# Optimization experiments

Hardware: AMD Instinct MI355X
Metric: run time of the kernel (lower is better)

Reference implementation:

```python
import jax, jax.numpy as jnp
import numpy as np

QN = 127.0  # 2^(8-1)-1, symmetric int8
EPS = 1e-5  # batchnorm eps

def ste_round(v):
    return v + jax.lax.stop_gradient(jnp.round(v) - v)

def quant_act(x):
    # HAWQ-style symmetric per-tensor activation quantization (8-bit)
    s = jnp.maximum(jnp.max(jnp.abs(x)) / QN, 1e-8)
    xq = jnp.clip(ste_round(x / s), -QN - 1.0, QN)
    return xq * s, s

def setup_inputs() -> dict:
    key = jax.random.key(0)
    k1, k2, k3, k4, k5, k6 = jax.random.split(key, 6)
    B, Cin, Cout, H, W = 128, 768, 192, 17, 17
    x = jax.random.normal(k1, (B, Cin, H, W), dtype=jnp.float32)
    conv_w = jax.random.normal(k2, (Cout, Cin, 1, 1), dtype=jnp.float32) * 0.02
    bn_gamma = 1.0 + 0.1 * jax.random.normal(k3, (Cout,), dtype=jnp.float32)
    bn_beta = 0.1 * jax.random.normal(k4, (Cout,), dtype=jnp.float32)
    bn_mean = 0.1 * jax.random.normal(k5, (Cout,), dtype=jnp.float32)
    bn_var = 0.5 + jax.random.uniform(k6, (Cout,), dtype=jnp.float32)
    return {"x": x, "conv_w": conv_w, "bn_gamma": bn_gamma, "bn_beta": bn_beta,
            "bn_mean": bn_mean, "bn_var": bn_var, "cluster": 0}

def reference(x, conv_w, bn_gamma, bn_beta, bn_mean, bn_var, cluster):
    # 1) QuantAct on raw input
    x1, s0 = quant_act(x)
    # 2) QuantAveragePool2d (k=3, s=1, p=1, count_include_pad=True): pool in integer domain
    x_int = ste_round(x1 / s0)
    pooled_sum = jax.lax.reduce_window(x_int, 0.0, jax.lax.add,
                                       (1, 1, 3, 3), (1, 1, 1, 1),
                                       [(0, 0), (0, 0), (1, 1), (1, 1)])
    x2 = (pooled_sum / 9.0) * s0
    # 3) QuantAct after pool
    x3, s1 = quant_act(x2)
    # 4) QuantBnConv2d: fold BN into 1x1 conv, per-channel symmetric weight quant
    std = jnp.sqrt(bn_var + EPS)
    w_fold = conv_w * (bn_gamma / std)[:, None, None, None]          # [O,C,1,1]
    b_fold = bn_beta - bn_gamma * bn_mean / std                      # [O]
    w_sf = jnp.maximum(jnp.max(jnp.abs(w_fold), axis=(1, 2, 3)) / QN, 1e-8)  # [O]
    w_int = jnp.clip(ste_round(w_fold / w_sf[:, None, None, None]), -QN - 1.0, QN)
    xi = x3 / s1                                                     # integer-valued acts
    b_int = ste_round(b_fold / (w_sf * s1))
    out_int = jnp.einsum('bchw,oc->bohw', xi, w_int[:, :, 0, 0]) + b_int[None, :, None, None]
    out = out_int * (w_sf * s1)[None, :, None, None]
    # 5) ReLU + output QuantAct
    out = jax.nn.relu(out)
    outq, s2 = quant_act(out)
    return outq, s2
```

## Files before the change

### kernel.cpp

```cpp
#include <hip/hip_runtime.h>
#include <math.h>

#define B_    128
#define C_    768
#define O_    192
#define HW_   289
#define N_IN  (128*768*289)
#define N_OUT (128*192*289)
#define QN_   127.0f

#define SLAB_E   (32*289)
#define SLAB_SH  9248
#define SLAB_BYT 18496
#define QP_LDS   (32*380)

#define AB_BLOCKS 2048

typedef __attribute__((ext_vector_type(4))) int i32x4;

#define SWZ(b) ((b) ^ ((((b) >> 6) & 3) << 4))


__global__ void k_pre(const float4* __restrict__ x4, int n4,
                      const float* __restrict__ conv_w,
                      const float* __restrict__ g,
                      const float* __restrict__ beta,
                      const float* __restrict__ mu,
                      const float* __restrict__ var,
                      signed char* __restrict__ w_q8,
                      float* __restrict__ wsf_g, float* __restrict__ bf_g,
                      unsigned* cnt) {
    if (blockIdx.x < AB_BLOCKS) {
        float m = 0.f;
        const int stride = AB_BLOCKS * blockDim.x;
        int i = blockIdx.x * blockDim.x + threadIdx.x;
        for (; i + stride < n4; i += 2 * stride) {
            float4 v = x4[i];
            float4 w = x4[i + stride];
            m = fmaxf(m, fmaxf(fmaxf(fabsf(v.x), fabsf(v.y)),
                               fmaxf(fabsf(v.z), fabsf(v.w))));
            m = fmaxf(m, fmaxf(fmaxf(fabsf(w.x), fabsf(w.y)),
                               fmaxf(fabsf(w.z), fabsf(w.w))));
        }
        if (i < n4) {
            float4 v = x4[i];
            m = fmaxf(m, fmaxf(fmaxf(fabsf(v.x), fabsf(v.y)),
                               fmaxf(fabsf(v.z), fabsf(v.w))));
        }
#pragma unroll
        for (int off = 32; off; off >>= 1) m = fmaxf(m, __shfl_down(m, off));
        __shared__ float sm[4];
        int lane = threadIdx.x & 63, wv = threadIdx.x >> 6;
        if (lane == 0) sm[wv] = m;
        __syncthreads();
        if (threadIdx.x == 0) {
            float bm = fmaxf(fmaxf(sm[0], sm[1]), fmaxf(sm[2], sm[3]));
            atomicMax(cnt + 0, __float_as_uint(bm));
        }
        return;
    }
    const int o = blockIdx.x - AB_BLOCKS;
    const float stdv = sqrtf(var[o] + 1e-5f);
    const float r = g[o] / stdv;
    const float* wo = conv_w + o * C_;
    float m = 0.f;
    for (int c = threadIdx.x; c < C_; c += 256) m = fmaxf(m, fabsf(wo[c] * r));
#pragma unroll
    for (int off = 32; off; off >>= 1) m = fmaxf(m, __shfl_down(m, off));
    __shared__ float sm2[4];
    __shared__ float swsf;
    int lane = threadIdx.x & 63, wv = threadIdx.x >> 6;
    if (lane == 0) sm2[wv] = m;
    __syncthreads();
    if (threadIdx.x == 0) {
        float bm = fmaxf(fmaxf(sm2[0], sm2[1]), fmaxf(sm2[2], sm2[3]));
        swsf = fmaxf(bm / QN_, 1e-8f);
    }
    __syncthreads();
    const float wsf = swsf;
    for (int c = threadIdx.x; c < C_; c += 256) {
        float wi = rintf(wo[c] * r / wsf);
        wi = fminf(fmaxf(wi, -128.f), 127.f);
        w_q8[(c >> 6) * 12288 + o * 64 + (c & 63)] = (signed char)(int)wi;
    }
    if (threadIdx.x == 0) {
        wsf_g[o] = wsf;
        bf_g[o] = beta[o] - g[o] * mu[o] / stdv;
    }
}

__launch_bounds__(512) __global__
void k_quant_pool(const float* __restrict__ x, short* __restrict__ pooled,
                  unsigned* cnt) {
    __shared__ __align__(16) float fq[QP_LDS + 8];
    __shared__ int smax[8];
    const int tid = threadIdx.x;
    const int kt = blockIdx.x;
    const int b = blockIdx.z;
    const float s0 = fmaxf(__uint_as_float(cnt[0]) / QN_, 1e-8f);

    for (int i = tid; i < 32 * 91; i += 512) {
        int p = i / 91, rem = i - p * 91;
        int slot;
        if (rem < 20) slot = rem;
        else if (rem < 40) slot = 360 + (rem - 20);
        else {
            int t = rem - 40;
            int rr = t / 3, cc = t - rr * 3;
            slot = (rr + 1) * 20 + (cc == 0 ? 0 : 17 + cc);
        }
        fq[p * 380 + slot] = 0.f;
    }
    if (tid < 8) fq[QP_LDS + tid] = 0.f;

    const float4* xg4 = (const float4*)(x + ((size_t)b * 768 + kt * 32) * HW_);
    for (int t = tid; t < SLAB_E / 4; t += 512) {
        float4 v = xg4[t];
        float q0 = rintf(v.x / s0);
        float q1 = rintf(v.y / s0);
        float q2 = rintf(v.z / s0);
        float q3 = rintf(v.w / s0);
        int e = 4 * t;
#pragma unroll
        for (int j = 0; j < 4; ++j) {
            float q = (j == 0) ? q0 : (j == 1) ? q1 : (j == 2) ? q2 : q3;
            int ej = e + j;
            int p = (ej * 29027) >> 23;
            int i2 = ej - p * 289;
            int r = (i2 * 3856) >> 16;
            int c = i2 - r * 17;
            fq[p * 380 + (r + 1) * 20 + (c + 1)] = q;
        }
    }
    __syncthreads();

    short* slab = pooled + (size_t)(b * 24 + kt) * SLAB_SH;
    int tmax = 0;
    for (int task = tid; task < 2720; task += 512) {
        int p = task & 31;
        int rt = task >> 5;
        int r = (rt * 3277) >> 14;
        int t5 = rt - r * 5;
        int c0 = t5 * 4;
        const float* base = fq + p * 380 + r * 20 + c0;
        float4 a0 = *(const float4*)(base);
        float4 a1 = *(const float4*)(base + 4);
        float4 b0 = *(const float4*)(base + 20);
        float4 b1 = *(const float4*)(base + 24);
        float4 d0 = *(const float4*)(base + 40);
        float4 d1 = *(const float4*)(base + 44);
        float s0c = a0.x + b0.x + d0.x;
        float s1c = a0.y + b0.y + d0.y;
        float s2c = a0.z + b0.z + d0.z;
        float s3c = a0.w + b0.w + d0.w;
        float s4c = a1.x + b1.x + d1.x;
        float s5c = a1.y + b1.y + d1.y;
        int o0 = (int)(s0c + s1c + s2c);
        int o1 = (int)(s1c + s2c + s3c);
        int o2 = (int)(s2c + s3c + s4c);
        int o3 = (int)(s3c + s4c + s5c);
        int i0 = r * 17 + c0;
        slab[(i0 + 0) * 32 + p] = (short)o0;
        int a = o0 < 0 ? -o0 : o0; tmax = a > tmax ? a : tmax;
        if (c0 + 1 < 17) {
            slab[(i0 + 1) * 32 + p] = (short)o1;
            a = o1 < 0 ? -o1 : o1; tmax = a > tmax ? a : tmax;
            slab[(i0 + 2) * 32 + p] = (short)o2;
            a = o2 < 0 ? -o2 : o2; tmax = a > tmax ? a : tmax;
            slab[(i0 + 3) * 32 + p] = (short)o3;
            a = o3 < 0 ? -o3 : o3; tmax = a > tmax ? a : tmax;
        }
    }

#pragma unroll
    for (int off = 32; off; off >>= 1) {
        int o = __shfl_down(tmax, off);
        tmax = o > tmax ? o : tmax;
    }
    if ((tid & 63) == 0) smax[tid >> 6] = tmax;
    __syncthreads();
    if (tid == 0) {
        int bm = smax[0];
#pragma unroll
        for (int i = 1; i < 8; ++i) bm = smax[i] > bm ? smax[i] : bm;
        atomicMax((int*)(cnt + 1), bm);
    }
}

__launch_bounds__(256) __global__
void k_gemm(const short* __restrict__ pooled,
            const signed char* __restrict__ w_q8,
            const float* __restrict__ wsf_g, const float* __restrict__ bf_g,
            unsigned* cnt, float* __restrict__ out) {
    __shared__ char sW[2][12288];
    __shared__ char sX[2][5120];
    __shared__ unsigned char s_lut[2305];
    __shared__ float s_bint[192];
    __shared__ float s_scale[192];
    __shared__ float red[4];
    const int tid = threadIdx.x;
    const int b = blockIdx.z;
    const int hw0 = blockIdx.x * 80;
    const int L = tid & 63;
    const int wv = tid >> 6;
    const int wo = wv * 48;
    const char* pooled_b = (const char*)pooled;

    {
        const float s0 = fmaxf(__uint_as_float(cnt[0]) / QN_, 1e-8f);
        const float maxx2 = ((float)((const int*)cnt)[1] / 9.0f) * s0;
        const float s1 = fmaxf(maxx2 / QN_, 1e-8f);
        for (int i = tid; i < 2305; i += 256) {
            float p = (float)(i - 1152);
            float t = (p / 9.0f) * s0;
            float v = rintf(t / s1);
            v = fminf(fmaxf(v, -128.f), 127.f);
            s_lut[i] = (unsigned char)(signed char)(int)v;
        }
        if (tid < 192) {
            float wsf = wsf_g[tid];
            s_bint[tid] = rintf(bf_g[tid] / (wsf * s1));
            s_scale[tid] = wsf * s1;
        }
    }

    const int row0 = tid >> 3, ch0 = tid & 7;
    const int row1 = 32 + (tid >> 3), ch1 = tid & 7;
    const int row2 = 64 + (tid >> 3), ch2 = tid & 7;
    const bool act2 = tid < 128;

    uint4 xr0, xr1, xr2;

    auto stageW = [&](int kt, int buf) {
#pragma unroll
        for (int j = 0; j < 3; ++j) {
            int ldsoff = (wv * 3 + j) * 1024;
            const char* src = (const char*)w_q8 + kt * 12288 + SWZ(ldsoff + L * 16);
            __builtin_amdgcn_global_load_lds(
                (const __attribute__((address_space(1))) unsigned int*)src,
                (__attribute__((address_space(3))) unsigned int*)(&sW[buf][0] + ldsoff),
                16, 0, 0);
        }
    };
    auto ldx = [&](int kt, int row, int ch) -> uint4 {
        uint4 z; z.x = z.y = z.z = z.w = 0u;
        int hw = hw0 + row;
        if (hw >= HW_) return z;
        size_t slab = (size_t)(b * 24 + 2 * kt + (ch >> 2)) * SLAB_BYT;
        return *(const uint4*)(pooled_b + slab + hw * 64 + (ch & 3) * 16);
    };
    auto loadX = [&](int kt) {
        xr0 = ldx(kt, row0, ch0);
        xr1 = ldx(kt, row1, ch1);
        if (act2) xr2 = ldx(kt, row2, ch2);
    };
    auto pack8 = [&](const uint4& v) -> uint2 {
        unsigned c0 = s_lut[1152 + (short)(v.x)];
        unsigned c1 = s_lut[1152 + (short)(v.x >> 16)];
        unsigned c2 = s_lut[1152 + (short)(v.y)];
        unsigned c3 = s_lut[1152 + (short)(v.y >> 16)];
        unsigned c4 = s_lut[1152 + (short)(v.z)];
        unsigned c5 = s_lut[1152 + (short)(v.z >> 16)];
        unsigned c6 = s_lut[1152 + (short)(v.w)];
        unsigned c7 = s_lut[1152 + (short)(v.w >> 16)];
        uint2 r;
        r.x = c0 | (c1 << 8) | (c2 << 16) | (c3 << 24);
        r.y = c4 | (c5 << 8) | (c6 << 16) | (c7 << 24);
        return r;
    };
    auto writeX = [&](int buf) {
        *(uint2*)(&sX[buf][0] + SWZ(row0 * 64 + ch0 * 8)) = pack8(xr0);
        *(uint2*)(&sX[buf][0] + SWZ(row1 * 64 + ch1 * 8)) = pack8(xr1);
        if (act2) *(uint2*)(&sX[buf][0] + SWZ(row2 * 64 + ch2 * 8)) = pack8(xr2);
    };

    i32x4 acc[3][5] = {};

    stageW(0, 0);
    loadX(0);
    __syncthreads();
    writeX(0);
    __syncthreads();

    for (int kt = 0; kt < 12; ++kt) {
        const int cur = kt & 1, nxt = cur ^ 1;
        if (kt < 11) {
            stageW(kt + 1, nxt);
            loadX(kt + 1);
        }
        i32x4 af[3], bfr[5];
#pragma unroll
        for (int m = 0; m < 3; ++m)
            af[m] = *(const i32x4*)(&sW[cur][0] +
                SWZ((wo + m * 16 + (L & 15)) * 64 + (L >> 4) * 16));
#pragma unroll
        for (int n = 0; n < 5; ++n)
            bfr[n] = *(const i32x4*)(&sX[cur][0] +
                SWZ((n * 16 + (L & 15)) * 64 + (L >> 4) * 16));
#pragma unroll
        for (int m = 0; m < 3; ++m)
#pragma unroll
            for (int n = 0; n < 5; ++n)
                acc[m][n] = __builtin_amdgcn_mfma_i32_16x16x64_i8(
                    af[m], bfr[n], acc[m][n], 0, 0, 0);
        if (kt < 11) writeX(nxt);
        __syncthreads();
    }

    float lmax = 0.f;
#pragma unroll
    for (int m = 0; m < 3; ++m) {
        int ob = wo + m * 16 + (L >> 4) * 4;
        float bi0 = s_bint[ob + 0], bi1 = s_bint[ob + 1];
        float bi2 = s_bint[ob + 2], bi3 = s_bint[ob + 3];
        float sc0 = s_scale[ob + 0], sc1 = s_scale[ob + 1];
        float sc2 = s_scale[ob + 2], sc3 = s_scale[ob + 3];
#pragma unroll
        for (int n = 0; n < 5; ++n) {
            int hw = hw0 + n * 16 + (L & 15);
            if (hw < HW_) {
                size_t base = ((size_t)b * O_ + ob) * HW_ + hw;
                float v0 = fmaxf(((float)acc[m][n][0] + bi0) * sc0, 0.f);
                float v1 = fmaxf(((float)acc[m][n][1] + bi1) * sc1, 0.f);
                float v2 = fmaxf(((float)acc[m][n][2] + bi2) * sc2, 0.f);
                float v3 = fmaxf(((float)acc[m][n][3] + bi3) * sc3, 0.f);
                out[base + 0 * HW_] = v0;
                out[base + 1 * HW_] = v1;
                out[base + 2 * HW_] = v2;
                out[base + 3 * HW_] = v3;
                lmax = fmaxf(fmaxf(fmaxf(v0, v1), fmaxf(v2, v3)), lmax);
            }
        }
    }
#pragma unroll
    for (int off = 32; off; off >>= 1) lmax = fmaxf(lmax, __shfl_down(lmax, off));
    if (L == 0) red[wv] = lmax;
    __syncthreads();
    if (tid == 0) {
        float bm = fmaxf(fmaxf(red[0], red[1]), fmaxf(red[2], red[3]));
        atomicMax(cnt + 2, __float_as_uint(bm));
    }
}

__global__ void k_quant_out(float* __restrict__ out, const unsigned* __restrict__ cnt) {
    const float s2 = fmaxf(__uint_as_float(cnt[2]) / QN_, 1e-8f);
    float4* o4 = (float4*)out;
    const int n4 = N_OUT / 4;
    for (int i = blockIdx.x * blockDim.x + threadIdx.x; i < n4;
         i += gridDim.x * blockDim.x) {
        float4 v = o4[i];
        v.x = fminf(fmaxf(rintf(v.x / s2), -128.f), 127.f) * s2;
        v.y = fminf(fmaxf(rintf(v.y / s2), -128.f), 127.f) * s2;
        v.z = fminf(fmaxf(rintf(v.z / s2), -128.f), 127.f) * s2;
        v.w = fminf(fmaxf(rintf(v.w / s2), -128.f), 127.f) * s2;
        o4[i] = v;
    }
    if (blockIdx.x == 0 && threadIdx.x == 0) out[N_OUT] = s2;
}

extern "C" void kernel_launch(void* const* d_in, const int* in_sizes, int n_in,
                              void* d_out, int out_size, void* d_ws, size_t ws_size,
                              hipStream_t stream) {
    const float* x      = (const float*)d_in[0];
    const float* conv_w = (const float*)d_in[1];
    const float* g      = (const float*)d_in[2];
    const float* beta   = (const float*)d_in[3];
    const float* mu     = (const float*)d_in[4];
    const float* var    = (const float*)d_in[5];
    float* out = (float*)d_out;

    char* wsb = (char*)d_ws;
    unsigned* cnt          = (unsigned*)wsb;
    float* wsf_g           = (float*)(wsb + 4096);
    float* bf_g            = (float*)(wsb + 5120);
    signed char* w_q8      = (signed char*)(wsb + 8192);
    short* pooled          = (short*)(wsb + (1u << 20));

    hipMemsetAsync(cnt, 0, 16, stream);
    k_pre<<<AB_BLOCKS + O_, 256, 0, stream>>>((const float4*)x, N_IN / 4, conv_w,
                                              g, beta, mu, var, w_q8, wsf_g, bf_g,
                                              cnt);
    dim3 qgrid(24, 1, B_);
    k_quant_pool<<<qgrid, 512, 0, stream>>>(x, pooled, cnt);
    dim3 ggrid(4, 1, B_);
    k_gemm<<<ggrid, 256, 0, stream>>>(pooled, w_q8, wsf_g, bf_g, cnt, out);
    k_quant_out<<<2048, 256, 0, stream>>>(out, cnt);
}
```

Baseline: 126.7 us.

## Split quant+pool into int8 quantize pass and separate LDS pool kernel

Replaces the fused quantize-and-pool kernel with two kernels. A grid-stride kernel quantizes x to int8 and writes it into the back half of each pooled slab. A second kernel loads that int8 slab into LDS and computes the 3x3 integer box sum with byte-unpacking and edge masking, writing int16 results in place. This shrinks LDS use and raises occupancy, at the cost of an extra launch and an extra global round trip of the int8 data, plus in-place aliasing between the int8 region and the int16 output.

```diff
diff --git a/kernel.cpp b/kernel.cpp
--- a/kernel.cpp
+++ b/kernel.cpp
@@ -9,11 +9,8 @@
 #define N_OUT (128*192*289)
 #define QN_   127.0f
 
-#define SLAB_E   (32*289)
 #define SLAB_SH  9248
 #define SLAB_BYT 18496
-#define QP_LDS   (32*380)
-
 #define AB_BLOCKS 2048
 
 typedef __attribute__((ext_vector_type(4))) int i32x4;
@@ -89,85 +86,114 @@
     }
 }
 
-__launch_bounds__(512) __global__
-void k_quant_pool(const float* __restrict__ x, short* __restrict__ pooled,
-                  unsigned* cnt) {
-    __shared__ __align__(16) float fq[QP_LDS + 8];
-    __shared__ int smax[8];
+__global__ void k_quant(const float4* __restrict__ x4, char* __restrict__ pbase,
+                        const unsigned* __restrict__ cnt) {
+    const float s0 = fmaxf(__uint_as_float(cnt[0]) / QN_, 1e-8f);
+    const int n4 = N_IN / 4;
+    for (int t = blockIdx.x * blockDim.x + threadIdx.x; t < n4;
+         t += gridDim.x * blockDim.x) {
+        float4 v = x4[t];
+        int q0 = (int)rintf(v.x / s0);
+        int q1 = (int)rintf(v.y / s0);
+        int q2 = (int)rintf(v.z / s0);
+        int q3 = (int)rintf(v.w / s0);
+        int e = 4 * t;
+        unsigned gp = (unsigned)e / 289u;
+        int hw = e - (int)gp * 289;
+        if (hw <= 285) {
+            size_t off = (size_t)(gp >> 5) * SLAB_BYT + 9248 + (gp & 31) * 289 + hw;
+            unsigned pk = (q0 & 0xff) | ((q1 & 0xff) << 8) | ((q2 & 0xff) << 16) |
+                          ((unsigned)(q3 & 0xff) << 24);
+            *(unsigned*)(pbase + off) = pk;
+        } else {
+            int qs0 = q0, qs1 = q1, qs2 = q2, qs3 = q3;
+#pragma unroll
+            for (int j = 0; j < 4; ++j) {
+                int qv = (j == 0) ? qs0 : (j == 1) ? qs1 : (j == 2) ? qs2 : qs3;
+                int ej = e + j;
+                unsigned gj = (unsigned)ej / 289u;
+                int hwj = ej - (int)gj * 289;
+                size_t oj = (size_t)(gj >> 5) * SLAB_BYT + 9248 + (gj & 31) * 289 + hwj;
+                pbase[oj] = (char)qv;
+            }
+        }
+    }
+}
+
+__launch_bounds__(256) __global__
+void k_pool(short* __restrict__ pooled, unsigned* cnt) {
+    __shared__ __align__(4) char sq[4 + 9248 + 12];
+    __shared__ int smax[4];
     const int tid = threadIdx.x;
-    const int kt = blockIdx.x;
-    const int b = blockIdx.z;
-    const float s0 = fmaxf(__uint_as_float(cnt[0]) / QN_, 1e-8f);
-
-    for (int i = tid; i < 32 * 91; i += 512) {
-        int p = i / 91, rem = i - p * 91;
-        int slot;
-        if (rem < 20) slot = rem;
-        else if (rem < 40) slot = 360 + (rem - 20);
-        else {
-            int t = rem - 40;
-            int rr = t / 3, cc = t - rr * 3;
-            slot = (rr + 1) * 20 + (cc == 0 ? 0 : 17 + cc);
-        }
-        fq[p * 380 + slot] = 0.f;
-    }
-    if (tid < 8) fq[QP_LDS + tid] = 0.f;
-
-    const float4* xg4 = (const float4*)(x + ((size_t)b * 768 + kt * 32) * HW_);
-    for (int t = tid; t < SLAB_E / 4; t += 512) {
-        float4 v = xg4[t];
-        float q0 = rintf(v.x / s0);
-        float q1 = rintf(v.y / s0);
-        float q2 = rintf(v.z / s0);
-        float q3 = rintf(v.w / s0);
-        int e = 4 * t;
-#pragma unroll
-        for (int j = 0; j < 4; ++j) {
-            float q = (j == 0) ? q0 : (j == 1) ? q1 : (j == 2) ? q2 : q3;
-            int ej = e + j;
-            int p = (ej * 29027) >> 23;
-            int i2 = ej - p * 289;
-            int r = (i2 * 3856) >> 16;
-            int c = i2 - r * 17;
-            fq[p * 380 + (r + 1) * 20 + (c + 1)] = q;
-        }
-    }
-    __syncthreads();
-
-    short* slab = pooled + (size_t)(b * 24 + kt) * SLAB_SH;
+    const int s = blockIdx.x;
+    char* region = (char*)pooled + (size_t)s * SLAB_BYT;
+
+    {
+        const unsigned* src = (const unsigned*)(region + 9248);
+        unsigned* dst = (unsigned*)(sq + 4);
+        for (int i = tid; i < 2312; i += 256) dst[i] = src[i];
+    }
+    if (tid < 4) *(unsigned*)(sq + tid * 4 * 0) = 0;
+    if (tid < 3) *(unsigned*)(sq + 4 + 9248 + tid * 4) = 0;
+    __syncthreads();
+
+    auto load6 = [&](int off, int& b0, int& b1, int& b2, int& b3, int& b4,
+                     int& b5) {
+        int al = off & ~3;
+        const char* base = sq + 4 + al;
+        unsigned w0 = *(const unsigned*)(base);
+        unsigned w1 = *(const unsigned*)(base + 4);
+        unsigned w2 = *(const unsigned*)(base + 8);
+        int sh = off & 3;
+        unsigned long long lo = (unsigned long long)w0 |
+                                ((unsigned long long)w1 << 32);
+        unsigned long long v = lo >> (8 * sh);
+        b0 = (int)(signed char)(v);
+        b1 = (int)(signed char)(v >> 8);
+        b2 = (int)(signed char)(v >> 16);
+        b3 = (int)(signed char)(v >> 24);
+        b4 = (int)(signed char)(v >> 32);
+        b5 = (sh == 3) ? (int)(signed char)w2 : (int)(signed char)(v >> 40);
+    };
+
+    short* slab16 = pooled + (size_t)s * SLAB_SH;
     int tmax = 0;
-    for (int task = tid; task < 2720; task += 512) {
+    for (int task = tid; task < 2720; task += 256) {
         int p = task & 31;
         int rt = task >> 5;
         int r = (rt * 3277) >> 14;
         int t5 = rt - r * 5;
         int c0 = t5 * 4;
-        const float* base = fq + p * 380 + r * 20 + c0;
-        float4 a0 = *(const float4*)(base);
-        float4 a1 = *(const float4*)(base + 4);
-        float4 b0 = *(const float4*)(base + 20);
-        float4 b1 = *(const float4*)(base + 24);
-        float4 d0 = *(const float4*)(base + 40);
-        float4 d1 = *(const float4*)(base + 44);
-        float s0c = a0.x + b0.x + d0.x;
-        float s1c = a0.y + b0.y + d0.y;
-        float s2c = a0.z + b0.z + d0.z;
-        float s3c = a0.w + b0.w + d0.w;
-        float s4c = a1.x + b1.x + d1.x;
-        float s5c = a1.y + b1.y + d1.y;
-        int o0 = (int)(s0c + s1c + s2c);
-        int o1 = (int)(s1c + s2c + s3c);
-        int o2 = (int)(s2c + s3c + s4c);
-        int o3 = (int)(s3c + s4c + s5c);
+        int rowbase = p * 289 + c0 - 1;
+        int cs0 = 0, cs1 = 0, cs2 = 0, cs3 = 0, cs4 = 0, cs5 = 0;
+        {
+            int b0, b1, b2, b3, b4, b5;
+            if (r > 0) {
+                load6(rowbase + (r - 1) * 17, b0, b1, b2, b3, b4, b5);
+                cs0 += b0; cs1 += b1; cs2 += b2; cs3 += b3; cs4 += b4; cs5 += b5;
+            }
+            load6(rowbase + r * 17, b0, b1, b2, b3, b4, b5);
+            cs0 += b0; cs1 += b1; cs2 += b2; cs3 += b3; cs4 += b4; cs5 += b5;
+            if (r < 16) {
+                load6(rowbase + (r + 1) * 17, b0, b1, b2, b3, b4, b5);
+                cs0 += b0; cs1 += b1; cs2 += b2; cs3 += b3; cs4 += b4; cs5 += b5;
+            }
+        }
+        if (c0 == 0) cs0 = 0;
+        if (c0 == 16) { cs2 = 0; cs3 = 0; cs4 = 0; cs5 = 0; }
+        int o0 = cs0 + cs1 + cs2;
+        int o1 = cs1 + cs2 + cs3;
+        int o2 = cs2 + cs3 + cs4;
+        int o3 = cs3 + cs4 + cs5;
         int i0 = r * 17 + c0;
-        slab[(i0 + 0) * 32 + p] = (short)o0;
+        slab16[(i0 + 0) * 32 + p] = (short)o0;
         int a = o0 < 0 ? -o0 : o0; tmax = a > tmax ? a : tmax;
         if (c0 + 1 < 17) {
-            slab[(i0 + 1) * 32 + p] = (short)o1;
+            slab16[(i0 + 1) * 32 + p] = (short)o1;
             a = o1 < 0 ? -o1 : o1; tmax = a > tmax ? a : tmax;
-            slab[(i0 + 2) * 32 + p] = (short)o2;
+            slab16[(i0 + 2) * 32 + p] = (short)o2;
             a = o2 < 0 ? -o2 : o2; tmax = a > tmax ? a : tmax;
-            slab[(i0 + 3) * 32 + p] = (short)o3;
+            slab16[(i0 + 3) * 32 + p] = (short)o3;
             a = o3 < 0 ? -o3 : o3; tmax = a > tmax ? a : tmax;
         }
     }
@@ -182,7 +208,7 @@
     if (tid == 0) {
         int bm = smax[0];
 #pragma unroll
-        for (int i = 1; i < 8; ++i) bm = smax[i] > bm ? smax[i] : bm;
+        for (int i = 1; i < 4; ++i) bm = smax[i] > bm ? smax[i] : bm;
         atomicMax((int*)(cnt + 1), bm);
     }
 }
@@ -380,8 +406,8 @@
     k_pre<<<AB_BLOCKS + O_, 256, 0, stream>>>((const float4*)x, N_IN / 4, conv_w,
                                               g, beta, mu, var, w_q8, wsf_g, bf_g,
                                               cnt);
-    dim3 qgrid(24, 1, B_);
-    k_quant_pool<<<qgrid, 512, 0, stream>>>(x, pooled, cnt);
+    k_quant<<<2048, 256, 0, stream>>>((const float4*)x, (char*)pooled, cnt);
+    k_pool<<<3072, 256, 0, stream>>>(pooled, cnt);
     dim3 ggrid(4, 1, B_);
     k_gemm<<<ggrid, 256, 0, stream>>>(pooled, w_q8, wsf_g, bf_g, cnt, out);
     k_quant_out<<<2048, 256, 0, stream>>>(out, cnt);
```

Result: slower. 155.4 us (+22.6%).
